# Kernel tuning notes

Hardware: AMD Instinct MI355X
Metric: run time of the kernel (lower is better)

The kernel has to match this reference:

```python
import jax, jax.numpy as jnp
import numpy as np

D = 256
H = 16
HD = D // H
N_BIAS = 6
B, E = 8, 1024


def _layernorm(x, g, b, eps=1e-5):
    mu = jnp.mean(x, axis=-1, keepdims=True)
    var = jnp.mean(jnp.square(x - mu), axis=-1, keepdims=True)
    return (x - mu) * jax.lax.rsqrt(var + eps) * g + b


def setup_inputs() -> dict:
    key = jax.random.key(0)
    ks = jax.random.split(key, 16)
    s = 0.02
    inp = {
        "x": jax.random.normal(ks[0], (B, E, D), dtype=jnp.float32),
        "struct_bias": jax.random.randint(ks[1], (B, E, E), 0, N_BIAS),
        "key_padding_mask": jnp.zeros((B, E), dtype=bool),
        # projections stored as [in, out] so y = x @ W + b
        "Wq": jax.random.normal(ks[2], (D, D), jnp.float32) * s,
        "bq": jnp.zeros((D,), jnp.float32),
        "Wk": jax.random.normal(ks[3], (D, D), jnp.float32) * s,
        "bk": jnp.zeros((D,), jnp.float32),
        "Wv": jax.random.normal(ks[4], (D, D), jnp.float32) * s,
        "bv": jnp.zeros((D,), jnp.float32),
        "Wo": jax.random.normal(ks[5], (D, D), jnp.float32) * s,
        "bo": jnp.zeros((D,), jnp.float32),
        "bias_emb": jax.random.normal(ks[6], (N_BIAS, H), jnp.float32) * s,
        "ln1_g": jnp.ones((D,), jnp.float32),
        "ln1_b": jnp.zeros((D,), jnp.float32),
        "W_ff1": jax.random.normal(ks[7], (D, 4 * D), jnp.float32) * s,
        "b_ff1": jnp.zeros((4 * D,), jnp.float32),
        "W_ff2": jax.random.normal(ks[8], (4 * D, D), jnp.float32) * s,
        "b_ff2": jnp.zeros((D,), jnp.float32),
        "ln2_g": jnp.ones((D,), jnp.float32),
        "ln2_b": jnp.zeros((D,), jnp.float32),
    }
    return inp


def reference(x, struct_bias, key_padding_mask, Wq, bq, Wk, bk, Wv, bv, Wo, bo,
              bias_emb, ln1_g, ln1_b, W_ff1, b_ff1, W_ff2, b_ff2, ln2_g, ln2_b):
    b, e, d = x.shape
    # project and split heads: [B, H, E, HD]
    q = (x @ Wq + bq).reshape(b, e, H, HD).transpose(0, 2, 1, 3)
    k = (x @ Wk + bk).reshape(b, e, H, HD).transpose(0, 2, 1, 3)
    v = (x @ Wv + bv).reshape(b, e, H, HD).transpose(0, 2, 1, 3)
    scores = jnp.einsum('bhqd,bhkd->bhqk', q, k) / np.sqrt(HD).astype(np.float32)
    # learned structural bias: [B,E,E,H] -> [B,H,E,E]
    bias = bias_emb[struct_bias].transpose(0, 3, 1, 2)
    scores = scores + bias
    scores = jnp.where(key_padding_mask[:, None, None, :], -jnp.inf, scores)
    attn = jax.nn.softmax(scores, axis=-1)
    out = jnp.einsum('bhqk,bhkd->bhqd', attn, v)
    out = out.transpose(0, 2, 1, 3).reshape(b, e, d)
    out = out @ Wo + bo
    x = _layernorm(x + out, ln1_g, ln1_b)
    ff = jax.nn.gelu(x @ W_ff1 + b_ff1, approximate=False) @ W_ff2 + b_ff2
    x = _layernorm(x + ff, ln2_g, ln2_b)
    return x
```

## Files before the change

### kernel.cpp

```cpp
#include <hip/hip_runtime.h>
#include <math.h>

#define B_  8
#define E_  1024
#define D_  256
#define H_  16
#define FF_ 1024
#define M_  (B_ * E_)

typedef __attribute__((ext_vector_type(8))) short short8;
typedef __attribute__((ext_vector_type(4))) float f32x4;
typedef unsigned short bf16u;

#define GLOAD_LDS16(g, l) __builtin_amdgcn_global_load_lds( \
    (const __attribute__((address_space(1))) void*)(g), \
    (__attribute__((address_space(3))) void*)(l), 16, 0, 0)

__device__ __forceinline__ unsigned short f2bf(float f) {
  union { float f; unsigned u; } c; c.f = f;
  unsigned r = c.u + 0x7fffu + ((c.u >> 16) & 1u);
  return (unsigned short)(r >> 16);
}
__device__ __forceinline__ float gelu_exact(float x) {
  return 0.5f * x * (1.0f + erff(x * 0.70710678118654752f));
}

template<int BM, int BN, int EPI>
__global__ __launch_bounds__(256) void mm_k(
    const bf16u* __restrict__ A, const bf16u* __restrict__ Wt,
    const float* __restrict__ bias, const float* __restrict__ R,
    void* __restrict__ Cout, int M, int N, int K)
{
  constexpr int WM = BM / 2, WN = BN / 2;
  constexpr int MT = WM / 16, NT = WN / 16;
  constexpr int PA = BM * 8 / 256, PB = BN * 8 / 256;
  constexpr int LBM = (BM == 128 ? 7 : 6), LBN = (BN == 128 ? 7 : 6);
  __shared__ bf16u As[BM * 64];
  __shared__ bf16u Bs[BN * 64];

  const int t = threadIdx.x;
  const int l15 = t & 15, quad = (t >> 4) & 3;
  const int w = t >> 6, wm = w >> 1, wn = w & 1;
  const int m0 = blockIdx.x * BM, n0 = blockIdx.y * BN;

  f32x4 acc[MT][NT];
  const f32x4 z4 = {0.f, 0.f, 0.f, 0.f};
#pragma unroll
  for (int i = 0; i < MT; ++i)
#pragma unroll
    for (int j = 0; j < NT; ++j) acc[i][j] = z4;

  for (int k0 = 0; k0 < K; k0 += 64) {
    __syncthreads();
#pragma unroll
    for (int p = 0; p < PA; ++p) {
      int g = p * 256 + t;
      int m = g & (BM - 1), c = g >> LBM;
      const bf16u* src = A + (size_t)(m0 + m) * K + k0 + c * 8;
      GLOAD_LDS16(src, As + g * 8);
    }
#pragma unroll
    for (int p = 0; p < PB; ++p) {
      int g = p * 256 + t;
      int n = g & (BN - 1), c = g >> LBN;
      const bf16u* src = Wt + (size_t)(n0 + n) * K + k0 + c * 8;
      GLOAD_LDS16(src, Bs + g * 8);
    }
    __syncthreads();
#pragma unroll
    for (int s = 0; s < 2; ++s) {
      short8 af[MT], bfr[NT];
#pragma unroll
      for (int mt = 0; mt < MT; ++mt)
        af[mt] = *(const short8*)(As + ((s * 4 + quad) * BM + wm * WM + mt * 16 + l15) * 8);
#pragma unroll
      for (int nt = 0; nt < NT; ++nt)
        bfr[nt] = *(const short8*)(Bs + ((s * 4 + quad) * BN + wn * WN + nt * 16 + l15) * 8);
#pragma unroll
      for (int mt = 0; mt < MT; ++mt)
#pragma unroll
        for (int nt = 0; nt < NT; ++nt)
          acc[mt][nt] = __builtin_amdgcn_mfma_f32_16x16x32_bf16(
              af[mt], bfr[nt], acc[mt][nt], 0, 0, 0);
    }
  }

#pragma unroll
  for (int mt = 0; mt < MT; ++mt) {
#pragma unroll
    for (int nt = 0; nt < NT; ++nt) {
      int col = n0 + wn * WN + nt * 16 + l15;
      float bia = bias[col];
#pragma unroll
      for (int r = 0; r < 4; ++r) {
        int row = m0 + wm * WM + mt * 16 + quad * 4 + r;
        float v = acc[mt][nt][r] + bia;
        if (EPI == 3) {
          size_t pidx = ((((size_t)(row >> 10) * 16 + ((col >> 4) & 15)) * 3 +
                          (col >> 8)) * E_ + (row & 1023)) * 16 + (col & 15);
          ((bf16u*)Cout)[pidx] = f2bf(v);
        } else {
          size_t idx = (size_t)row * N + col;
          if (EPI == 1)      { ((float*)Cout)[idx] = v + R[idx]; }
          else if (EPI == 2) { ((bf16u*)Cout)[idx] = f2bf(gelu_exact(v)); }
          else               { ((bf16u*)Cout)[idx] = f2bf(v); }
        }
      }
    }
  }
}

__global__ __launch_bounds__(256) void prep_k(
    const float* __restrict__ Wq, const float* __restrict__ Wk,
    const float* __restrict__ Wv, const float* __restrict__ Wo,
    const float* __restrict__ Wf1, const float* __restrict__ Wf2,
    bf16u* __restrict__ Wqkvt, bf16u* __restrict__ Wot,
    bf16u* __restrict__ Wf1t, bf16u* __restrict__ Wf2t,
    const float* __restrict__ bq, const float* __restrict__ bk,
    const float* __restrict__ bv, float* __restrict__ bqkv,
    const float* __restrict__ X, bf16u* __restrict__ Xb)
{
  __shared__ float tile[32][33];
  const int gid = blockIdx.x;
  const int t = threadIdx.x;

  if (gid < 768) {
    const float* src; bf16u* dst; int K, N, bx, by;
    if (gid < 256) {
      const int z = gid >> 6, r = gid & 63;
      src = (z == 0) ? Wq : (z == 1) ? Wk : (z == 2) ? Wv : Wo;
      dst = (z == 0) ? Wqkvt : (z == 1) ? Wqkvt + 65536
          : (z == 2) ? Wqkvt + 131072 : Wot;
      K = 256; N = 256; bx = r & 7; by = r >> 3;
    } else if (gid < 512) {
      const int r = gid - 256;
      src = Wf1; dst = Wf1t; K = 256; N = 1024; bx = r & 7; by = r >> 3;
    } else {
      const int r = gid - 512;
      src = Wf2; dst = Wf2t; K = 1024; N = 256; bx = r & 31; by = r >> 5;
    }
    const int tx = t & 31, ty = t >> 5;
    const int kb = bx * 32, nb = by * 32;
#pragma unroll
    for (int r = 0; r < 4; ++r)
      tile[ty + 8 * r][tx] = src[(size_t)(kb + ty + 8 * r) * N + nb + tx];
    __syncthreads();
#pragma unroll
    for (int r = 0; r < 4; ++r)
      dst[(size_t)(nb + ty + 8 * r) * K + kb + tx] = f2bf(tile[tx][ty + 8 * r]);
  } else if (gid < 771) {
    int i = (gid - 768) * 256 + t;
    bqkv[i] = (i < 256) ? bq[i] : (i < 512) ? bk[i - 256] : bv[i - 512];
  } else {
    int i = (gid - 771) * 256 + t;
    float4 a = ((const float4*)X)[i * 2];
    float4 b = ((const float4*)X)[i * 2 + 1];
    uint4 o;
    o.x = f2bf(a.x) | ((unsigned)f2bf(a.y) << 16);
    o.y = f2bf(a.z) | ((unsigned)f2bf(a.w) << 16);
    o.z = f2bf(b.x) | ((unsigned)f2bf(b.y) << 16);
    o.w = f2bf(b.z) | ((unsigned)f2bf(b.w) << 16);
    ((uint4*)Xb)[i] = o;
  }
}

__global__ __launch_bounds__(256) void attn_k(
    const bf16u* __restrict__ qkv, const int* __restrict__ sb,
    const unsigned char* __restrict__ mask, const float* __restrict__ be,
    bf16u* __restrict__ O)
{
  __shared__ bf16u Kl[2][2][64][16];
  __shared__ bf16u Vt[2][2][2][16][40];
  __shared__ float emb2[6][2];

  const int t    = threadIdx.x;
  const int b    = blockIdx.z;
  const int hg   = blockIdx.y;
  const int w    = t >> 6;
  const int lane = t & 63;
  const int l15  = lane & 15;
  const int quad = lane >> 4;
  const int q0w  = blockIdx.x * 64 + w * 16;
  const float C2 = 0.36067376022224085f;

  if (t < 12) emb2[t >> 1][t & 1] = be[(t >> 1) * 16 + hg * 2 + (t & 1)] * 1.44269504088896f;

  short8 qf[2];
#pragma unroll
  for (int hp = 0; hp < 2; ++hp) {
    uint4 v = {0u, 0u, 0u, 0u};
    if (quad < 2)
      v = *(const uint4*)(qkv +
          ((((size_t)b * 16 + hg * 2 + hp) * 3 + 0) * E_ + q0w + l15) * 16 + quad * 8);
    union { uint4 u; short8 s; } c; c.u = v;
    qf[hp] = c.s;
  }

  const int s_hp   = t >> 7;
  const int s_key  = (t >> 1) & 63;
  const int s_half = t & 1;
  const int vu     = t & 127;
  const int vz     = vu >> 2;
  const int vh     = (vu >> 1) & 1;
  const int vjh    = vu & 1;
  const int vs2    = vz >> 4;
  const int vrow0  = vh * 8 + vjh * 4;
  const int vc     = ((vz >> 1) & 3) * 8 + ((vz >> 3) & 1) * 4 + (vz & 1) * 2;

  const bf16u* kbase = qkv + (((size_t)b * 16 + hg * 2 + s_hp) * 3 + 1) * E_ * 16 + s_half * 8;
  const bf16u* vbase = qkv + (((size_t)b * 16 + hg * 2 + s_hp) * 3 + 2) * E_ * 16 + vrow0;
  const int* sbp = sb + ((size_t)(b * E_) + q0w + l15) * E_;
  const unsigned char* maskp = mask + (size_t)b * E_;

  f32x4 accO[2];
  const f32x4 z4 = {0.f, 0.f, 0.f, 0.f};
  accO[0] = z4; accO[1] = z4;
  float lsum[2] = {0.f, 0.f};

  uint4 kA;
  uint2 va, vb;
  int sraw[2][2][4];
  unsigned mvA[2][2];
  {
    kA = *(const uint4*)(kbase + (size_t)s_key * 16);
    const bf16u* p0 = vbase + (size_t)(2 * vz) * 16;
    va = *(const uint2*)p0;
    vb = *(const uint2*)(p0 + 16);
#pragma unroll
    for (int s2 = 0; s2 < 2; ++s2)
#pragma unroll
      for (int kb2 = 0; kb2 < 2; ++kb2) {
        *(int4*)&sraw[s2][kb2][0] =
            *(const int4*)(sbp + s2 * 32 + kb2 * 16 + quad * 4);
        mvA[s2][kb2] = *(const unsigned*)(maskp + s2 * 32 + kb2 * 16 + quad * 4);
      }
  }
  __syncthreads();

#pragma unroll 2
  for (int i = 0; i < 16; ++i) {
    const int cur = i & 1;

    *(uint4*)&Kl[cur][s_hp][s_key][s_half * 8] = kA;
    {
      union { uint2 u; bf16u e[4]; } a, c; a.u = va; c.u = vb;
#pragma unroll
      for (int j = 0; j < 4; ++j)
        *(unsigned*)&Vt[cur][s_hp][vs2][vrow0 + j][vc] =
            (unsigned)a.e[j] | ((unsigned)c.e[j] << 16);
    }

    __syncthreads();

    int srn[2][2][4];
    unsigned mvN[2][2];
    if (i < 15) {
      const int kn = (i + 1) * 64;
      kA = *(const uint4*)(kbase + (size_t)(kn + s_key) * 16);
      const bf16u* p0 = vbase + (size_t)(kn + 2 * vz) * 16;
      va = *(const uint2*)p0;
      vb = *(const uint2*)(p0 + 16);
#pragma unroll
      for (int s2 = 0; s2 < 2; ++s2)
#pragma unroll
        for (int kb2 = 0; kb2 < 2; ++kb2) {
          *(int4*)&srn[s2][kb2][0] =
              *(const int4*)(sbp + kn + s2 * 32 + kb2 * 16 + quad * 4);
          mvN[s2][kb2] = *(const unsigned*)(maskp + kn + s2 * 32 + kb2 * 16 + quad * 4);
        }
    }

    __builtin_amdgcn_s_setprio(1);
#pragma unroll
    for (int s2 = 0; s2 < 2; ++s2) {
      union { uint4 u; short8 s; } kc00, kc01, kc10, kc11;
      kc00.u = (uint4){0u,0u,0u,0u}; kc01.u = (uint4){0u,0u,0u,0u};
      kc10.u = (uint4){0u,0u,0u,0u}; kc11.u = (uint4){0u,0u,0u,0u};
      if (quad < 2) {
        kc00.u = *(const uint4*)&Kl[cur][0][s2 * 32 + l15][quad * 8];
        kc01.u = *(const uint4*)&Kl[cur][0][s2 * 32 + 16 + l15][quad * 8];
        kc10.u = *(const uint4*)&Kl[cur][1][s2 * 32 + l15][quad * 8];
        kc11.u = *(const uint4*)&Kl[cur][1][s2 * 32 + 16 + l15][quad * 8];
      }
      f32x4 sc00 = __builtin_amdgcn_mfma_f32_16x16x32_bf16(kc00.s, qf[0], z4, 0, 0, 0);
      f32x4 sc01 = __builtin_amdgcn_mfma_f32_16x16x32_bf16(kc01.s, qf[0], z4, 0, 0, 0);
      f32x4 sc10 = __builtin_amdgcn_mfma_f32_16x16x32_bf16(kc10.s, qf[1], z4, 0, 0, 0);
      f32x4 sc11 = __builtin_amdgcn_mfma_f32_16x16x32_bf16(kc11.s, qf[1], z4, 0, 0, 0);

      unsigned pk0[4], pk1[4];
#pragma unroll
      for (int r = 0; r < 4; ++r) {
        float2 w0 = *(const float2*)&emb2[sraw[s2][0][r]][0];
        float2 w1 = *(const float2*)&emb2[sraw[s2][1][r]][0];
        float p00 = __builtin_amdgcn_exp2f(fmaf(sc00[r], C2, w0.x));
        float p01 = __builtin_amdgcn_exp2f(fmaf(sc01[r], C2, w1.x));
        float p10 = __builtin_amdgcn_exp2f(fmaf(sc10[r], C2, w0.y));
        float p11 = __builtin_amdgcn_exp2f(fmaf(sc11[r], C2, w1.y));
        unsigned mb0 = (mvA[s2][0] >> (r * 8)) & 0xffu;
        unsigned mb1 = (mvA[s2][1] >> (r * 8)) & 0xffu;
        p00 = mb0 ? 0.f : p00;  p10 = mb0 ? 0.f : p10;
        p01 = mb1 ? 0.f : p01;  p11 = mb1 ? 0.f : p11;
        unsigned u00 = __float_as_uint(p00), u01 = __float_as_uint(p01);
        unsigned u10 = __float_as_uint(p10), u11 = __float_as_uint(p11);
        lsum[0] += __uint_as_float(u00 & 0xffff0000u) + __uint_as_float(u01 & 0xffff0000u);
        lsum[1] += __uint_as_float(u10 & 0xffff0000u) + __uint_as_float(u11 & 0xffff0000u);
        if ((r & 1) == 0) {
          pk0[r >> 1]       = u00 >> 16;
          pk0[2 + (r >> 1)] = u01 >> 16;
          pk1[r >> 1]       = u10 >> 16;
          pk1[2 + (r >> 1)] = u11 >> 16;
        } else {
          pk0[r >> 1]       |= u00 & 0xffff0000u;
          pk0[2 + (r >> 1)] |= u01 & 0xffff0000u;
          pk1[r >> 1]       |= u10 & 0xffff0000u;
          pk1[2 + (r >> 1)] |= u11 & 0xffff0000u;
        }
      }
      union { unsigned u[4]; short8 s; } a0, a1;
      a0.u[0] = pk0[0]; a0.u[1] = pk0[1]; a0.u[2] = pk0[2]; a0.u[3] = pk0[3];
      a1.u[0] = pk1[0]; a1.u[1] = pk1[1]; a1.u[2] = pk1[2]; a1.u[3] = pk1[3];

      short8 vf0 = *(const short8*)&Vt[cur][0][s2][l15][quad * 8];
      short8 vf1 = *(const short8*)&Vt[cur][1][s2][l15][quad * 8];
      accO[0] = __builtin_amdgcn_mfma_f32_16x16x32_bf16(a0.s, vf0, accO[0], 0, 0, 0);
      accO[1] = __builtin_amdgcn_mfma_f32_16x16x32_bf16(a1.s, vf1, accO[1], 0, 0, 0);
    }
    __builtin_amdgcn_s_setprio(0);

    if (i < 15) {
#pragma unroll
      for (int s2 = 0; s2 < 2; ++s2)
#pragma unroll
        for (int kb2 = 0; kb2 < 2; ++kb2) {
#pragma unroll
          for (int r = 0; r < 4; ++r)
            sraw[s2][kb2][r] = srn[s2][kb2][r];
          mvA[s2][kb2] = mvN[s2][kb2];
        }
    }
  }

#pragma unroll
  for (int hp = 0; hp < 2; ++hp) {
    lsum[hp] += __shfl_xor(lsum[hp], 16, 64);
    lsum[hp] += __shfl_xor(lsum[hp], 32, 64);
  }
#pragma unroll
  for (int hp = 0; hp < 2; ++hp) {
#pragma unroll
    for (int r = 0; r < 4; ++r) {
      float lq = __shfl(lsum[hp], quad * 4 + r, 64);
      float o = accO[hp][r] / lq;
      O[((size_t)(b * E_) + q0w + quad * 4 + r) * 256 + (hg * 2 + hp) * 16 + l15] = f2bf(o);
    }
  }
}

template<int DUAL>
__global__ __launch_bounds__(256) void ln_k(
    const float* __restrict__ X, const float* __restrict__ g,
    const float* __restrict__ bta, float* __restrict__ Y, bf16u* __restrict__ Yb)
{
  const int row  = blockIdx.x * 4 + (threadIdx.x >> 6);
  const int lane = threadIdx.x & 63;
  float4 v = *(const float4*)(X + (size_t)row * D_ + lane * 4);
  float s  = v.x + v.y + v.z + v.w;
  float ss = v.x * v.x + v.y * v.y + v.z * v.z + v.w * v.w;
#pragma unroll
  for (int off = 32; off; off >>= 1) {
    s  += __shfl_xor(s, off, 64);
    ss += __shfl_xor(ss, off, 64);
  }
  float mu  = s * (1.f / 256.f);
  float var = ss * (1.f / 256.f) - mu * mu;
  float rs  = 1.f / sqrtf(var + 1e-5f);
  float4 gv = *(const float4*)(g + lane * 4);
  float4 bv = *(const float4*)(bta + lane * 4);
  float4 o;
  o.x = (v.x - mu) * rs * gv.x + bv.x;
  o.y = (v.y - mu) * rs * gv.y + bv.y;
  o.z = (v.z - mu) * rs * gv.z + bv.z;
  o.w = (v.w - mu) * rs * gv.w + bv.w;
  *(float4*)(Y + (size_t)row * D_ + lane * 4) = o;
  if (DUAL) {
    uint2 p;
    p.x = f2bf(o.x) | ((unsigned)f2bf(o.y) << 16);
    p.y = f2bf(o.z) | ((unsigned)f2bf(o.w) << 16);
    *(uint2*)(Yb + (size_t)row * D_ + lane * 4) = p;
  }
}

extern "C" void kernel_launch(void* const* d_in, const int* in_sizes, int n_in,
                              void* d_out, int out_size, void* d_ws, size_t ws_size,
                              hipStream_t stream) {
  const float* x   = (const float*)d_in[0];
  const int*   sb  = (const int*)d_in[1];
  const unsigned char* mask = (const unsigned char*)d_in[2];
  const float* Wq  = (const float*)d_in[3];
  const float* bq  = (const float*)d_in[4];
  const float* Wk  = (const float*)d_in[5];
  const float* bk  = (const float*)d_in[6];
  const float* Wv  = (const float*)d_in[7];
  const float* bv  = (const float*)d_in[8];
  const float* Wo  = (const float*)d_in[9];
  const float* bo  = (const float*)d_in[10];
  const float* be  = (const float*)d_in[11];
  const float* g1  = (const float*)d_in[12];
  const float* b1  = (const float*)d_in[13];
  const float* Wf1 = (const float*)d_in[14];
  const float* bf1 = (const float*)d_in[15];
  const float* Wf2 = (const float*)d_in[16];
  const float* bf2 = (const float*)d_in[17];
  const float* g2  = (const float*)d_in[18];
  const float* b2  = (const float*)d_in[19];
  float* out = (float*)d_out;

  char* ws = (char*)d_ws;
  bf16u* Wqkvt = (bf16u*)(ws + 0);
  bf16u* Wot   = (bf16u*)(ws + 393216);
  bf16u* Wf1t  = (bf16u*)(ws + 524288);
  bf16u* Wf2t  = (bf16u*)(ws + 1048576);
  float* bqkv  = (float*)(ws + 1572864);
  bf16u* xb    = (bf16u*)(ws + 2097152);
  bf16u* qkv   = (bf16u*)(ws + 6291456);
  bf16u* att   = (bf16u*)(ws + 18874368);
  float* t1    = (float*)(ws + 23068672);
  float* x1    = (float*)(ws + 31457280);
  bf16u* x1b   = (bf16u*)(ws + 39845888);
  bf16u* ffh   = (bf16u*)(ws + 2097152);
  float* t2    = (float*)(ws + 18874368);

  dim3 blk(256);

  prep_k<<<1795, blk, 0, stream>>>(Wq, Wk, Wv, Wo, Wf1, Wf2,
                                   Wqkvt, Wot, Wf1t, Wf2t,
                                   bq, bk, bv, bqkv, x, xb);

  mm_k<128, 128, 3><<<dim3(64, 6), blk, 0, stream>>>(xb, Wqkvt, bqkv, nullptr,
                                                     qkv, M_, 768, 256);
  attn_k<<<dim3(16, 8, 8), blk, 0, stream>>>(qkv, sb, mask, be, att);

  mm_k<128, 64, 1><<<dim3(64, 4), blk, 0, stream>>>(att, Wot, bo, x,
                                                    t1, M_, 256, 256);
  ln_k<1><<<M_ / 4, blk, 0, stream>>>(t1, g1, b1, x1, x1b);

  mm_k<128, 128, 2><<<dim3(64, 8), blk, 0, stream>>>(x1b, Wf1t, bf1, nullptr,
                                                     ffh, M_, 1024, 256);
  mm_k<128, 64, 1><<<dim3(64, 4), blk, 0, stream>>>(ffh, Wf2t, bf2, x1,
                                                    t2, M_, 256, 1024);
  ln_k<0><<<M_ / 4, blk, 0, stream>>>(t2, g2, b2, out, nullptr);
}
```

Measured before the change: 239.9 us.

## Fuse residual+LayerNorm into output GEMMs and fold key mask into MFMA

The two residual-add plus LayerNorm steps move into the epilogues of the Wo and FF2 GEMMs. These use 32x256 tiles so each block holds full rows and reduces mean and variance through shuffles and shared memory, which removes the separate LN kernels and the fp32 round trips through t1 and t2. In attention, the key-padding mask is injected as an extra K/Q dot-product term inside the QK MFMA (a large negative bf16 value times 1.0), replacing the per-element select. The QKV GEMM tile also changes to 64x128. The trade-off is that the small-BM GEMM tiles may reuse data less and run at lower occupancy.

```diff
diff --git a/kernel.cpp b/kernel.cpp
--- a/kernel.cpp
+++ b/kernel.cpp
@@ -29,14 +29,18 @@
 __global__ __launch_bounds__(256) void mm_k(
     const bf16u* __restrict__ A, const bf16u* __restrict__ Wt,
     const float* __restrict__ bias, const float* __restrict__ R,
-    void* __restrict__ Cout, int M, int N, int K)
+    void* __restrict__ Cout, int M, int N, int K,
+    const float* __restrict__ lng, const float* __restrict__ lnb,
+    bf16u* __restrict__ Cb)
 {
   constexpr int WM = BM / 2, WN = BN / 2;
   constexpr int MT = WM / 16, NT = WN / 16;
   constexpr int PA = BM * 8 / 256, PB = BN * 8 / 256;
-  constexpr int LBM = (BM == 128 ? 7 : 6), LBN = (BN == 128 ? 7 : 6);
+  constexpr int LBM = (BM == 128 ? 7 : BM == 64 ? 6 : 5);
+  constexpr int LBN = (BN == 256 ? 8 : BN == 128 ? 7 : 6);
   __shared__ bf16u As[BM * 64];
   __shared__ bf16u Bs[BN * 64];
+  __shared__ float red[2][2][16][2];
 
   const int t = threadIdx.x;
   const int l15 = t & 15, quad = (t >> 4) & 3;
@@ -83,6 +87,56 @@
           acc[mt][nt] = __builtin_amdgcn_mfma_f32_16x16x32_bf16(
               af[mt], bfr[nt], acc[mt][nt], 0, 0, 0);
     }
+  }
+
+  if (EPI == 4 || EPI == 5) {
+    float s[4] = {0.f, 0.f, 0.f, 0.f}, ss[4] = {0.f, 0.f, 0.f, 0.f};
+#pragma unroll
+    for (int nt = 0; nt < NT; ++nt) {
+      int col = n0 + wn * WN + nt * 16 + l15;
+      float bia = bias[col];
+#pragma unroll
+      for (int r = 0; r < 4; ++r) {
+        int row = m0 + wm * WM + quad * 4 + r;
+        float v = acc[0][nt][r] + bia + R[(size_t)row * N + col];
+        acc[0][nt][r] = v;
+        s[r] += v; ss[r] += v * v;
+      }
+    }
+#pragma unroll
+    for (int off = 1; off <= 8; off <<= 1)
+#pragma unroll
+      for (int r = 0; r < 4; ++r) {
+        s[r]  += __shfl_xor(s[r], off, 64);
+        ss[r] += __shfl_xor(ss[r], off, 64);
+      }
+    if (l15 == 0) {
+#pragma unroll
+      for (int r = 0; r < 4; ++r) {
+        red[wm][wn][quad * 4 + r][0] = s[r];
+        red[wm][wn][quad * 4 + r][1] = ss[r];
+      }
+    }
+    __syncthreads();
+#pragma unroll
+    for (int r = 0; r < 4; ++r) {
+      int row16 = quad * 4 + r;
+      float st  = red[wm][0][row16][0] + red[wm][1][row16][0];
+      float sst = red[wm][0][row16][1] + red[wm][1][row16][1];
+      float mu  = st * (1.f / 256.f);
+      float var = sst * (1.f / 256.f) - mu * mu;
+      float rs  = 1.f / sqrtf(var + 1e-5f);
+      int row = m0 + wm * WM + row16;
+#pragma unroll
+      for (int nt = 0; nt < NT; ++nt) {
+        int col = n0 + wn * WN + nt * 16 + l15;
+        float o = (acc[0][nt][r] - mu) * rs * lng[col] + lnb[col];
+        size_t idx = (size_t)row * N + col;
+        ((float*)Cout)[idx] = o;
+        if (EPI == 4) Cb[idx] = f2bf(o);
+      }
+    }
+    return;
   }
 
 #pragma unroll
@@ -192,6 +246,8 @@
     if (quad < 2)
       v = *(const uint4*)(qkv +
           ((((size_t)b * 16 + hg * 2 + hp) * 3 + 0) * E_ + q0w + l15) * 16 + quad * 8);
+    else if (quad == 2)
+      v.x = 0x3F80u;
     union { uint4 u; short8 s; } c; c.u = v;
     qf[hp] = c.s;
   }
@@ -220,7 +276,7 @@
   uint4 kA;
   uint2 va, vb;
   int sraw[2][2][4];
-  unsigned mvA[2][2];
+  bf16u mkA[2][2];
   {
     kA = *(const uint4*)(kbase + (size_t)s_key * 16);
     const bf16u* p0 = vbase + (size_t)(2 * vz) * 16;
@@ -232,7 +288,7 @@
       for (int kb2 = 0; kb2 < 2; ++kb2) {
         *(int4*)&sraw[s2][kb2][0] =
             *(const int4*)(sbp + s2 * 32 + kb2 * 16 + quad * 4);
-        mvA[s2][kb2] = *(const unsigned*)(maskp + s2 * 32 + kb2 * 16 + quad * 4);
+        mkA[s2][kb2] = maskp[s2 * 32 + kb2 * 16 + l15] ? (bf16u)0xCF6E : (bf16u)0;
       }
   }
   __syncthreads();
@@ -253,7 +309,7 @@
     __syncthreads();
 
     int srn[2][2][4];
-    unsigned mvN[2][2];
+    bf16u mkN[2][2];
     if (i < 15) {
       const int kn = (i + 1) * 64;
       kA = *(const uint4*)(kbase + (size_t)(kn + s_key) * 16);
@@ -266,16 +322,20 @@
         for (int kb2 = 0; kb2 < 2; ++kb2) {
           *(int4*)&srn[s2][kb2][0] =
               *(const int4*)(sbp + kn + s2 * 32 + kb2 * 16 + quad * 4);
-          mvN[s2][kb2] = *(const unsigned*)(maskp + kn + s2 * 32 + kb2 * 16 + quad * 4);
+          mkN[s2][kb2] = maskp[kn + s2 * 32 + kb2 * 16 + l15] ? (bf16u)0xCF6E : (bf16u)0;
         }
     }
 
     __builtin_amdgcn_s_setprio(1);
 #pragma unroll
     for (int s2 = 0; s2 < 2; ++s2) {
+      unsigned inj0 = (quad == 2) ? (unsigned)mkA[s2][0] : 0u;
+      unsigned inj1 = (quad == 2) ? (unsigned)mkA[s2][1] : 0u;
       union { uint4 u; short8 s; } kc00, kc01, kc10, kc11;
-      kc00.u = (uint4){0u,0u,0u,0u}; kc01.u = (uint4){0u,0u,0u,0u};
-      kc10.u = (uint4){0u,0u,0u,0u}; kc11.u = (uint4){0u,0u,0u,0u};
+      kc00.u = (uint4){inj0, 0u, 0u, 0u};
+      kc01.u = (uint4){inj1, 0u, 0u, 0u};
+      kc10.u = (uint4){inj0, 0u, 0u, 0u};
+      kc11.u = (uint4){inj1, 0u, 0u, 0u};
       if (quad < 2) {
         kc00.u = *(const uint4*)&Kl[cur][0][s2 * 32 + l15][quad * 8];
         kc01.u = *(const uint4*)&Kl[cur][0][s2 * 32 + 16 + l15][quad * 8];
@@ -296,10 +356,6 @@
         float p01 = __builtin_amdgcn_exp2f(fmaf(sc01[r], C2, w1.x));
         float p10 = __builtin_amdgcn_exp2f(fmaf(sc10[r], C2, w0.y));
         float p11 = __builtin_amdgcn_exp2f(fmaf(sc11[r], C2, w1.y));
-        unsigned mb0 = (mvA[s2][0] >> (r * 8)) & 0xffu;
-        unsigned mb1 = (mvA[s2][1] >> (r * 8)) & 0xffu;
-        p00 = mb0 ? 0.f : p00;  p10 = mb0 ? 0.f : p10;
-        p01 = mb1 ? 0.f : p01;  p11 = mb1 ? 0.f : p11;
         unsigned u00 = __float_as_uint(p00), u01 = __float_as_uint(p01);
         unsigned u10 = __float_as_uint(p10), u11 = __float_as_uint(p11);
         lsum[0] += __uint_as_float(u00 & 0xffff0000u) + __uint_as_float(u01 & 0xffff0000u);
@@ -335,7 +391,7 @@
 #pragma unroll
           for (int r = 0; r < 4; ++r)
             sraw[s2][kb2][r] = srn[s2][kb2][r];
-          mvA[s2][kb2] = mvN[s2][kb2];
+          mkA[s2][kb2] = mkN[s2][kb2];
         }
     }
   }
@@ -353,40 +409,6 @@
       float o = accO[hp][r] / lq;
       O[((size_t)(b * E_) + q0w + quad * 4 + r) * 256 + (hg * 2 + hp) * 16 + l15] = f2bf(o);
     }
-  }
-}
-
-template<int DUAL>
-__global__ __launch_bounds__(256) void ln_k(
-    const float* __restrict__ X, const float* __restrict__ g,
-    const float* __restrict__ bta, float* __restrict__ Y, bf16u* __restrict__ Yb)
-{
-  const int row  = blockIdx.x * 4 + (threadIdx.x >> 6);
-  const int lane = threadIdx.x & 63;
-  float4 v = *(const float4*)(X + (size_t)row * D_ + lane * 4);
-  float s  = v.x + v.y + v.z + v.w;
-  float ss = v.x * v.x + v.y * v.y + v.z * v.z + v.w * v.w;
-#pragma unroll
-  for (int off = 32; off; off >>= 1) {
-    s  += __shfl_xor(s, off, 64);
-    ss += __shfl_xor(ss, off, 64);
-  }
-  float mu  = s * (1.f / 256.f);
-  float var = ss * (1.f / 256.f) - mu * mu;
-  float rs  = 1.f / sqrtf(var + 1e-5f);
-  float4 gv = *(const float4*)(g + lane * 4);
-  float4 bv = *(const float4*)(bta + lane * 4);
-  float4 o;
-  o.x = (v.x - mu) * rs * gv.x + bv.x;
-  o.y = (v.y - mu) * rs * gv.y + bv.y;
-  o.z = (v.z - mu) * rs * gv.z + bv.z;
-  o.w = (v.w - mu) * rs * gv.w + bv.w;
-  *(float4*)(Y + (size_t)row * D_ + lane * 4) = o;
-  if (DUAL) {
-    uint2 p;
-    p.x = f2bf(o.x) | ((unsigned)f2bf(o.y) << 16);
-    p.y = f2bf(o.z) | ((unsigned)f2bf(o.w) << 16);
-    *(uint2*)(Yb + (size_t)row * D_ + lane * 4) = p;
   }
 }
 
@@ -424,11 +446,9 @@
   bf16u* xb    = (bf16u*)(ws + 2097152);
   bf16u* qkv   = (bf16u*)(ws + 6291456);
   bf16u* att   = (bf16u*)(ws + 18874368);
-  float* t1    = (float*)(ws + 23068672);
   float* x1    = (float*)(ws + 31457280);
   bf16u* x1b   = (bf16u*)(ws + 39845888);
   bf16u* ffh   = (bf16u*)(ws + 2097152);
-  float* t2    = (float*)(ws + 18874368);
 
   dim3 blk(256);
 
@@ -436,17 +456,15 @@
                                    Wqkvt, Wot, Wf1t, Wf2t,
                                    bq, bk, bv, bqkv, x, xb);
 
-  mm_k<128, 128, 3><<<dim3(64, 6), blk, 0, stream>>>(xb, Wqkvt, bqkv, nullptr,
-                                                     qkv, M_, 768, 256);
+  mm_k<64, 128, 3><<<dim3(128, 6), blk, 0, stream>>>(
+      xb, Wqkvt, bqkv, nullptr, qkv, M_, 768, 256, nullptr, nullptr, nullptr);
   attn_k<<<dim3(16, 8, 8), blk, 0, stream>>>(qkv, sb, mask, be, att);
 
-  mm_k<128, 64, 1><<<dim3(64, 4), blk, 0, stream>>>(att, Wot, bo, x,
-                                                    t1, M_, 256, 256);
-  ln_k<1><<<M_ / 4, blk, 0, stream>>>(t1, g1, b1, x1, x1b);
-
-  mm_k<128, 128, 2><<<dim3(64, 8), blk, 0, stream>>>(x1b, Wf1t, bf1, nullptr,
-                                                     ffh, M_, 1024, 256);
-  mm_k<128, 64, 1><<<dim3(64, 4), blk, 0, stream>>>(ffh, Wf2t, bf2, x1,
-                                                    t2, M_, 256, 1024);
-  ln_k<0><<<M_ / 4, blk, 0, stream>>>(t2, g2, b2, out, nullptr);
-}
+  mm_k<32, 256, 4><<<dim3(256, 1), blk, 0, stream>>>(
+      att, Wot, bo, x, x1, M_, 256, 256, g1, b1, x1b);
+
+  mm_k<128, 128, 2><<<dim3(64, 8), blk, 0, stream>>>(
+      x1b, Wf1t, bf1, nullptr, ffh, M_, 1024, 256, nullptr, nullptr, nullptr);
+  mm_k<32, 256, 5><<<dim3(256, 1), blk, 0, stream>>>(
+      ffh, Wf2t, bf2, x1, out, M_, 256, 1024, g2, b2, nullptr);
+}
```

Result: slower. 251.2 us (+4.7%).
